# Performance work log

Hardware: AMD Instinct MI355X
Metric: run time of the kernel (lower is better)

The kernel has to match this reference:

```python
import jax, jax.numpy as jnp
import numpy as np

FILTER = [1.0, 3.0, 3.0, 1.0]  # filter_type
PAD = 1  # padding on each side


def _blur_kernel():
    k = jnp.asarray(FILTER, dtype=jnp.float32)
    kernel = jnp.outer(k, k)          # direction='vh' -> 4x4
    kernel = kernel / kernel.sum()
    return kernel


def setup_inputs() -> dict:
    key = jax.random.key(0)
    h = jax.random.normal(key, (8, 256, 64, 512), dtype=jnp.float32)
    return {"h": h}


def reference(h):
    # Pad: horizontal circular (ring=True), then vertical reflect.
    hp = jnp.pad(h, ((0, 0), (0, 0), (0, 0), (PAD, PAD)), mode='wrap')
    hp = jnp.pad(hp, ((0, 0), (0, 0), (PAD, PAD), (0, 0)), mode='reflect')
    C = h.shape[1]
    kernel = _blur_kernel()  # (4,4)
    # Depthwise conv: one 4x4 filter per channel (groups=C).
    w = jnp.broadcast_to(kernel[None, None], (C, 1, 4, 4))  # OIHW, I=1
    out = jax.lax.conv_general_dilated(
        hp, w,
        window_strides=(1, 1),
        padding='VALID',
        dimension_numbers=('NCHW', 'OIHW', 'NCHW'),
        feature_group_count=C,
    )
    return out  # (B, C, H-1, W-1) for 4x4 kernel with pad 1, stride 1
```

## Files before the change

kernel.cpp:

```cpp
#include <hip/hip_runtime.h>


constexpr int H_ = 64, W_ = 512;
constexpr int HO = 63, WO = 511;
constexpr int GROUPS = W_ / 4;
constexpr int NCHUNK = 4, CHUNK = 16;

__device__ __forceinline__ int rowmap(int p) {
    int r = p - 1;
    if (p == 0)  r = 1;
    if (p > H_)  r = H_ - 2;
    return r;
}

__device__ __forceinline__ float4 hblur_row(const float* __restrict__ row,
                                            int c0, int pcol, int bcol) {
    const float4 A  = *reinterpret_cast<const float4*>(row + c0);
    const float2 Bv = *reinterpret_cast<const float2*>(row + bcol);
    const float  p  = row[pcol];
    float4 r;
    r.x = fmaf(3.f, A.x + A.y, p   + A.z);
    r.y = fmaf(3.f, A.y + A.z, A.x + A.w);
    r.z = fmaf(3.f, A.z + A.w, A.y + Bv.x);
    r.w = fmaf(3.f, A.w + Bv.x, A.z + Bv.y);
    return r;
}

__global__ __launch_bounds__(256) void blur_kernel(const float* __restrict__ h,
                                                   float* __restrict__ out) {
    const int tid   = blockIdx.x * blockDim.x + threadIdx.x;
    const int g     = tid & (GROUPS - 1);
    const int chunk = (tid >> 7) & (NCHUNK - 1);
    const int bc    = tid >> 9;

    const float* img = h   + (size_t)bc * (H_ * W_);
    float*       op  = out + (size_t)bc * (HO * WO);

    const int c0   = g * 4;
    const int pcol = (c0 - 1) & (W_ - 1);
    const int bcol = (c0 + 4) & (W_ - 1);

    const int oy0 = chunk * CHUNK;
    const int R   = min(CHUNK, HO - oy0);

    float4 h0 = hblur_row(img + rowmap(oy0)     * W_, c0, pcol, bcol);
    float4 h1 = hblur_row(img + rowmap(oy0 + 1) * W_, c0, pcol, bcol);
    float4 h2 = hblur_row(img + rowmap(oy0 + 2) * W_, c0, pcol, bcol);

    const int nstore = (g == GROUPS - 1) ? 3 : 4;

    #pragma unroll 4
    for (int j = 0; j < R; ++j) {
        const int p3 = oy0 + j + 3;
        const float4 h3 = hblur_row(img + rowmap(p3) * W_, c0, pcol, bcol);

        float o[4];
        o[0] = (h0.x + h3.x + 3.f * (h1.x + h2.x)) * (1.f / 64.f);
        o[1] = (h0.y + h3.y + 3.f * (h1.y + h2.y)) * (1.f / 64.f);
        o[2] = (h0.z + h3.z + 3.f * (h1.z + h2.z)) * (1.f / 64.f);
        o[3] = (h0.w + h3.w + 3.f * (h1.w + h2.w)) * (1.f / 64.f);

        float* dst = op + (size_t)(oy0 + j) * WO + c0;
        #pragma unroll
        for (int k = 0; k < 4; ++k)
            if (k < nstore) __builtin_nontemporal_store(o[k], dst + k);

        h0 = h1; h1 = h2; h2 = h3;
    }
}

extern "C" void kernel_launch(void* const* d_in, const int* in_sizes, int n_in,
                              void* d_out, int out_size, void* d_ws, size_t ws_size,
                              hipStream_t stream) {
    const float* h = (const float*)d_in[0];
    float* out = (float*)d_out;

    const int total = 2048 * NCHUNK * GROUPS;
    const int block = 256;
    const int grid  = total / block;
    blur_kernel<<<grid, block, 0, stream>>>(h, out);
}
```

Before: 498.0 us.

## Use one wavefront per row band with 8 columns per lane and shuffle halos

```diff
diff --git a/kernel.cpp b/kernel.cpp
--- a/kernel.cpp
+++ b/kernel.cpp
@@ -3,8 +3,9 @@
 
 constexpr int H_ = 64, W_ = 512;
 constexpr int HO = 63, WO = 511;
-constexpr int GROUPS = W_ / 4;
-constexpr int NCHUNK = 4, CHUNK = 16;
+constexpr int CHUNK = 16;
+
+struct F8 { float v[8]; };
 
 __device__ __forceinline__ int rowmap(int p) {
     int r = p - 1;
@@ -13,58 +14,50 @@
     return r;
 }
 
-__device__ __forceinline__ float4 hblur_row(const float* __restrict__ row,
-                                            int c0, int pcol, int bcol) {
-    const float4 A  = *reinterpret_cast<const float4*>(row + c0);
-    const float2 Bv = *reinterpret_cast<const float2*>(row + bcol);
-    const float  p  = row[pcol];
-    float4 r;
-    r.x = fmaf(3.f, A.x + A.y, p   + A.z);
-    r.y = fmaf(3.f, A.y + A.z, A.x + A.w);
-    r.z = fmaf(3.f, A.z + A.w, A.y + Bv.x);
-    r.w = fmaf(3.f, A.w + Bv.x, A.z + Bv.y);
-    return r;
+__device__ __forceinline__ F8 hblur_row(const float* __restrict__ row, int lane) {
+    const float4 Va = *reinterpret_cast<const float4*>(row + 8 * lane);
+    const float4 Vb = *reinterpret_cast<const float4*>(row + 8 * lane + 4);
+    const float left = __shfl(Vb.w, (lane + 63) & 63, 64);
+    const float r0   = __shfl(Va.x, (lane + 1) & 63, 64);
+    const float r1   = __shfl(Va.y, (lane + 1) & 63, 64);
+    const float x[11] = {left, Va.x, Va.y, Va.z, Va.w,
+                         Vb.x, Vb.y, Vb.z, Vb.w, r0, r1};
+    F8 o;
+    #pragma unroll
+    for (int i = 0; i < 8; ++i)
+        o.v[i] = fmaf(3.f, x[i + 1] + x[i + 2], x[i] + x[i + 3]);
+    return o;
 }
 
 __global__ __launch_bounds__(256) void blur_kernel(const float* __restrict__ h,
                                                    float* __restrict__ out) {
     const int tid   = blockIdx.x * blockDim.x + threadIdx.x;
-    const int g     = tid & (GROUPS - 1);
-    const int chunk = (tid >> 7) & (NCHUNK - 1);
-    const int bc    = tid >> 9;
+    const int lane  = tid & 63;
+    const int wid   = tid >> 6;
+    const int band  = wid & 3;
+    const int bc    = wid >> 2;
 
     const float* img = h   + (size_t)bc * (H_ * W_);
     float*       op  = out + (size_t)bc * (HO * WO);
 
-    const int c0   = g * 4;
-    const int pcol = (c0 - 1) & (W_ - 1);
-    const int bcol = (c0 + 4) & (W_ - 1);
+    const int oy0 = (band < 3) ? band * CHUNK : HO - CHUNK;
 
-    const int oy0 = chunk * CHUNK;
-    const int R   = min(CHUNK, HO - oy0);
+    F8 h0 = hblur_row(img + rowmap(oy0)     * W_, lane);
+    F8 h1 = hblur_row(img + rowmap(oy0 + 1) * W_, lane);
+    F8 h2 = hblur_row(img + rowmap(oy0 + 2) * W_, lane);
 
-    float4 h0 = hblur_row(img + rowmap(oy0)     * W_, c0, pcol, bcol);
-    float4 h1 = hblur_row(img + rowmap(oy0 + 1) * W_, c0, pcol, bcol);
-    float4 h2 = hblur_row(img + rowmap(oy0 + 2) * W_, c0, pcol, bcol);
-
-    const int nstore = (g == GROUPS - 1) ? 3 : 4;
+    const int ncol = (lane == 63) ? 7 : 8;
 
     #pragma unroll 4
-    for (int j = 0; j < R; ++j) {
-        const int p3 = oy0 + j + 3;
-        const float4 h3 = hblur_row(img + rowmap(p3) * W_, c0, pcol, bcol);
-
-        float o[4];
-        o[0] = (h0.x + h3.x + 3.f * (h1.x + h2.x)) * (1.f / 64.f);
-        o[1] = (h0.y + h3.y + 3.f * (h1.y + h2.y)) * (1.f / 64.f);
-        o[2] = (h0.z + h3.z + 3.f * (h1.z + h2.z)) * (1.f / 64.f);
-        o[3] = (h0.w + h3.w + 3.f * (h1.w + h2.w)) * (1.f / 64.f);
-
-        float* dst = op + (size_t)(oy0 + j) * WO + c0;
+    for (int j = 0; j < CHUNK; ++j) {
+        const F8 h3 = hblur_row(img + rowmap(oy0 + j + 3) * W_, lane);
+        float* dst = op + (size_t)(oy0 + j) * WO + 8 * lane;
         #pragma unroll
-        for (int k = 0; k < 4; ++k)
-            if (k < nstore) __builtin_nontemporal_store(o[k], dst + k);
-
+        for (int i = 0; i < 8; ++i) {
+            const float o =
+                (h0.v[i] + h3.v[i] + 3.f * (h1.v[i] + h2.v[i])) * (1.f / 64.f);
+            if (i < ncol) dst[i] = o;
+        }
         h0 = h1; h1 = h2; h2 = h3;
     }
 }
@@ -75,7 +68,7 @@
     const float* h = (const float*)d_in[0];
     float* out = (float*)d_out;
 
-    const int total = 2048 * NCHUNK * GROUPS;
+    const int total = 2048 * 4 * 64;
     const int block = 256;
     const int grid  = total / block;
     blur_kernel<<<grid, block, 0, stream>>>(h, out);
```

Measured after the change: 459.1 us. 7.8% less time.
